# Performance work log

Measured on AMD Instinct MI355X. Metric: run time of the kernel, lower is better.

Reference implementation:

```python
import jax, jax.numpy as jnp
import numpy as np

NEG_INF_SCALE = -1e9


def setup_inputs() -> dict:
    key = jax.random.key(0)
    ks = jax.random.split(key, 8)
    B, T, M, D = 64, 1024, 256, 1024
    query = jax.random.normal(ks[0], (B, 1, M), dtype=jnp.float32)
    keys = jax.random.normal(ks[1], (B, T, M), dtype=jnp.float32)
    values = jax.random.normal(ks[2], (B, T, D), dtype=jnp.float32)
    mask = jax.random.randint(ks[3], (B, 1, T), 0, 2).astype(jnp.float32)
    # MLP params (scaled like torch default init ~ 1/sqrt(fan_in))
    W1 = jax.random.normal(ks[4], (4 * M, D), dtype=jnp.float32) / np.sqrt(4 * M)
    b1 = jnp.zeros((D,), dtype=jnp.float32)
    W2 = jax.random.normal(ks[5], (D, D), dtype=jnp.float32) / np.sqrt(D)
    b2 = jnp.zeros((D,), dtype=jnp.float32)
    w_score = jax.random.normal(ks[6], (D, 1), dtype=jnp.float32) / np.sqrt(D)
    b_score = jnp.zeros((1,), dtype=jnp.float32)
    return {"query": query, "keys": keys, "values": values, "mask": mask,
            "W1": W1, "b1": b1, "W2": W2, "b2": b2,
            "w_score": w_score, "b_score": b_score}


def reference(query, keys, values, mask, W1, b1, W2, b2, w_score, b_score):
    # query: [B,1,M] broadcast against keys: [B,T,M]
    q = jnp.broadcast_to(query, keys.shape)
    att_input = jnp.concatenate([q, keys, q - keys, q * keys], axis=-1)  # [B,T,4M]
    h = jax.nn.relu(att_input @ W1 + b1)   # [B,T,D]
    h = jax.nn.relu(h @ W2 + b2)           # [B,T,D]
    score = h @ w_score + b_score          # [B,T,1]
    logits = jnp.swapaxes(score, 1, 2)     # [B,1,T]
    logits = logits + mask * NEG_INF_SCALE
    attn = jax.nn.softmax(logits, axis=-1)  # [B,1,T]
    out = jnp.matmul(attn, values)          # [B,1,D]
    return out
```

## Files before the change

### kernel.cpp

```cpp
#include <hip/hip_runtime.h>

#define DEV __device__ __forceinline__

typedef __attribute__((ext_vector_type(4))) float f32x4;
typedef __attribute__((ext_vector_type(8))) short short8;
typedef __attribute__((ext_vector_type(4))) short s16x4;
typedef __attribute__((ext_vector_type(4))) float f32x4v;

DEV short f2bf(float f) {
  union { float f; unsigned u; } v; v.f = f;
  unsigned r = (v.u + 0x7FFFu + ((v.u >> 16) & 1u)) >> 16;
  return (short)r;
}

DEV void gload16(const void* g, void* l) {
  __builtin_amdgcn_global_load_lds(
      (const __attribute__((address_space(1))) void*)g,
      (__attribute__((address_space(3))) void*)l, 16, 0, 0);
}

#define BAR() __builtin_amdgcn_s_barrier()
#define LGKMW(n)                                              \
  {                                                           \
    asm volatile("s_waitcnt lgkmcnt(" #n ")" ::: "memory");   \
    __builtin_amdgcn_sched_barrier(0);                        \
  }
#define VMW(n)                                                \
  {                                                           \
    asm volatile("s_waitcnt vmcnt(" #n ")" ::: "memory");     \
    __builtin_amdgcn_sched_barrier(0);                        \
  }


__global__ __launch_bounds__(256) void k_prep_all(
    const float* __restrict__ keys, const float* __restrict__ w2,
    const float* __restrict__ w1, const float* __restrict__ query,
    const float* __restrict__ b1, short* __restrict__ keysb,
    short* __restrict__ w2f, short* __restrict__ wktf,
    float* __restrict__ biasb) {
  __shared__ __align__(16) char smem[45056];
  const int bid = blockIdx.x;
  const int tid = threadIdx.x;

  if (bid < 256) {
    short (*tile)[64][72] = (short (*)[64][72])(smem);
    float (*qlds)[256] = (float (*)[256])(smem + 36864);
    float (*redm)[64][4] = (float (*)[64][4])(smem + 40960);
    const int r = bid;
    const int bg = r & 15, d0g = r >> 4, d0 = d0g * 64;
    const int d = tid & 63, mq = tid >> 6;

    for (int idx = tid; idx < 1024; idx += 256)
      qlds[idx >> 8][idx & 255] = query[(bg * 4 + (idx >> 8)) * 256 + (idx & 255)];
    __syncthreads();

    float bacc[4] = {0.f, 0.f, 0.f, 0.f};
    const int l = tid & 63, cgl = tid >> 6;

    for (int mc = 0; mc < 4; ++mc) {
#pragma unroll 4
      for (int i = 0; i < 16; ++i) {
        int ml = i * 4 + mq;
        int m = mc * 64 + ml;
        float wa = w1[(size_t)m * 1024 + d0 + d];
        float wb = w1[(size_t)(256 + m) * 1024 + d0 + d];
        float wc = w1[(size_t)(512 + m) * 1024 + d0 + d];
        float wd = w1[(size_t)(768 + m) * 1024 + d0 + d];
        float bc = wb - wc, ac = wa + wc;
#pragma unroll
        for (int bb = 0; bb < 4; ++bb) {
          float qv = qlds[bb][m];
          tile[bb][d][ml] = f2bf(bc + qv * wd);
          bacc[bb] += qv * ac;
        }
      }
      __syncthreads();
#pragma unroll
      for (int bb = 0; bb < 4; ++bb) {
        short* ob = wktf + (size_t)(bg * 4 + bb) * 262144;
#pragma unroll
        for (int kh = 0; kh < 2; ++kh) {
          short8 v = *(const short8*)&tile[bb][cgl * 16 + (l & 15)]
                                          [kh * 32 + (l >> 4) * 8];
          *(short8*)&ob[((size_t)((mc * 2 + kh) * 64 + d0g * 4 + cgl)) * 512 + l * 8] = v;
        }
      }
      __syncthreads();
    }

    redm[0][d][mq] = bacc[0];
    redm[1][d][mq] = bacc[1];
    redm[2][d][mq] = bacc[2];
    redm[3][d][mq] = bacc[3];
    __syncthreads();
    const int bb = tid >> 6, dd = tid & 63;
    biasb[(bg * 4 + bb) * 1024 + d0 + dd] =
        redm[bb][dd][0] + redm[bb][dd][1] + redm[bb][dd][2] + redm[bb][dd][3] +
        b1[d0 + dd];
  } else if (bid < 512) {
    float (*tile)[65] = (float (*)[65])(smem);
    const int r = bid - 256;
    const int kt = r & 15, n0 = (r >> 4) * 64;
    const int a = tid & 63, q = tid >> 6;
#pragma unroll
    for (int i = 0; i < 16; ++i) {
      int kk = i * 4 + q;
      tile[kk][a] = w2[(size_t)(kt * 64 + kk) * 1024 + n0 + a];
    }
    __syncthreads();
    const int l = tid & 63, cgl = tid >> 6;
#pragma unroll
    for (int kh = 0; kh < 2; ++kh) {
      short8 v;
#pragma unroll
      for (int j = 0; j < 8; ++j)
        v[j] = f2bf(tile[kh * 32 + (l >> 4) * 8 + j][cgl * 16 + (l & 15)]);
      *(short8*)&w2f[((size_t)((kt * 2 + kh) * 64 + (n0 >> 4) + cgl)) * 512 + l * 8] = v;
    }
  } else {
    int i = ((bid - 512) * 256 + tid) * 8;
    f32x4v v0 = *(const f32x4v*)(keys + i);
    f32x4v v1 = *(const f32x4v*)(keys + i + 4);
    short8 s;
    s[0] = f2bf(v0[0]); s[1] = f2bf(v0[1]); s[2] = f2bf(v0[2]); s[3] = f2bf(v0[3]);
    s[4] = f2bf(v1[0]); s[5] = f2bf(v1[1]); s[6] = f2bf(v1[2]); s[7] = f2bf(v1[3]);
    *(short8*)(keysb + i) = s;
  }
}


template <int MODE>
__global__ __launch_bounds__(256, 3) void k_gemm(const short* __restrict__ A,
                                                 const short* __restrict__ Bf,
                                                 const float* __restrict__ bias,
                                                 const float* __restrict__ wscore,
                                                 short* __restrict__ hout,
                                                 float* __restrict__ spart) {
  __shared__ short lds[12288];
  constexpr int SK = (MODE == 1) ? 256 : 1024;
  constexpr int KT = (MODE == 1) ? 4 : 16;

  const int tid = threadIdx.x;
  const int bx = blockIdx.x;
  const int L = (bx & 7) * 512 + (bx >> 3);

  const short *Ab, *Bb;
  const float *biasp, *wsp = nullptr;
  short* houtp = nullptr;
  int rt, ct;
  if constexpr (MODE == 1) {
    const int b = L >> 6;
    rt = (L >> 2) & 15; ct = L & 3;
    Ab = A + ((size_t)(b * 1024 + rt * 64)) * 256;
    Bb = Bf + (size_t)b * 262144;
    biasp = bias + b * 1024 + ct * 256;
    houtp = hout + ((size_t)(b * 1024 + rt * 64)) * 1024 + ct * 256;
  } else {
    rt = L >> 2; ct = L & 3;
    Ab = A + (size_t)rt * 64 * 1024;
    Bb = Bf;
    biasp = bias + ct * 256;
    wsp = wscore + ct * 256;
  }

  int gA[2], dA[2];
#pragma unroll
  for (int j = 0; j < 2; ++j) {
    int s = tid + j * 256, row = s >> 3, kc = (s & 7) ^ (row & 7);
    gA[j] = row * SK + kc * 8;
    dA[j] = s * 8;
  }
  auto STAGE = [&](int kt) {
    const int bb = (kt % 3) * 4096;
#pragma unroll
    for (int j = 0; j < 2; ++j) gload16(Ab + gA[j] + kt * 64, &lds[bb + dA[j]]);
  };

  const int lane = tid & 63, l15 = lane & 15, l4 = lane >> 4, wc = tid >> 6;
  const int afo0 = l15 * 64 + ((l4 ^ (l15 & 7)) * 8);
  const int afo1 = l15 * 64 + (((4 + l4) ^ (l15 & 7)) * 8);

  f32x4 acc[4][4];
#pragma unroll
  for (int m = 0; m < 4; ++m)
#pragma unroll
    for (int n = 0; n < 4; ++n) acc[m][n] = f32x4{0.f, 0.f, 0.f, 0.f};
  short8 bf[4];
  short8 af[4];

#define LOADB(kt, kh_)                                                          \
  _Pragma("unroll") for (int n_ = 0; n_ < 4; ++n_) {                            \
    bf[n_] = *(const short8*)(Bb +                                              \
        ((size_t)(((kt) * 2 + (kh_)) * 64 + ct * 16 + wc * 4 + n_) << 9) +      \
        lane * 8);                                                              \
  }

  STAGE(0);
  STAGE(1);
  VMW(2);
  BAR();

#pragma unroll
  for (int t = 0; t < KT; ++t) {
    const int bb = (t % 3) * 4096;
    LOADB(t, 0);
#pragma unroll
    for (int m = 0; m < 4; ++m) af[m] = *(const short8*)&lds[bb + afo0 + m * 1024];
    LGKMW(0);
    __builtin_amdgcn_s_setprio(1);
#pragma unroll
    for (int m = 0; m < 4; ++m)
#pragma unroll
      for (int n = 0; n < 4; ++n)
        acc[m][n] = __builtin_amdgcn_mfma_f32_16x16x32_bf16(bf[n], af[m],
                                                            acc[m][n], 0, 0, 0);
    __builtin_amdgcn_s_setprio(0);
    LOADB(t, 1);
    if (t + 2 < KT) STAGE(t + 2);
#pragma unroll
    for (int m = 0; m < 4; ++m) af[m] = *(const short8*)&lds[bb + afo1 + m * 1024];
    LGKMW(0);
    __builtin_amdgcn_s_setprio(1);
#pragma unroll
    for (int m = 0; m < 4; ++m)
#pragma unroll
      for (int n = 0; n < 4; ++n)
        acc[m][n] = __builtin_amdgcn_mfma_f32_16x16x32_bf16(bf[n], af[m],
                                                            acc[m][n], 0, 0, 0);
    __builtin_amdgcn_s_setprio(0);
    if (t + 2 < KT) {
      VMW(2);
    } else {
      VMW(0);
    }
    BAR();
  }
#undef LOADB

  if constexpr (MODE == 1) {
    float bv[4][4];
#pragma unroll
    for (int n = 0; n < 4; ++n)
#pragma unroll
      for (int r2 = 0; r2 < 4; ++r2)
        bv[n][r2] = biasp[wc * 64 + n * 16 + l4 * 4 + r2];
#pragma unroll
    for (int m = 0; m < 4; ++m) {
      int row = m * 16 + l15;
#pragma unroll
      for (int n = 0; n < 4; ++n) {
        s16x4 pk;
#pragma unroll
        for (int r2 = 0; r2 < 4; ++r2)
          pk[r2] = f2bf(fmaxf(acc[m][n][r2] + bv[n][r2], 0.f));
        *(s16x4*)&houtp[(size_t)row * 1024 + wc * 64 + n * 16 + l4 * 4] = pk;
      }
    }
  } else {
    float bv[4][4], wv[4][4];
#pragma unroll
    for (int n = 0; n < 4; ++n)
#pragma unroll
      for (int r2 = 0; r2 < 4; ++r2) {
        int c = wc * 64 + n * 16 + l4 * 4 + r2;
        bv[n][r2] = biasp[c];
        wv[n][r2] = wsp[c];
      }
    float* so = spart + ((size_t)(ct * 4 + wc) << 16) + rt * 64;
#pragma unroll
    for (int m = 0; m < 4; ++m) {
      float s = 0.f;
#pragma unroll
      for (int n = 0; n < 4; ++n)
#pragma unroll
        for (int r2 = 0; r2 < 4; ++r2)
          s += fmaxf(acc[m][n][r2] + bv[n][r2], 0.f) * wv[n][r2];
      s += __shfl_xor(s, 16);
      s += __shfl_xor(s, 32);
      if (lane < 16) so[m * 16 + l15] = s;
    }
  }
}

__global__ __launch_bounds__(256) void k_out(const float* __restrict__ spart,
                                             const float* __restrict__ mask,
                                             const float* __restrict__ bscore,
                                             const float* __restrict__ values,
                                             float* __restrict__ part) {
  const int b = blockIdx.x >> 3, ts = blockIdx.x & 7;
  const int tid = threadIdx.x;
  __shared__ float sm[1024];
  __shared__ float red[8];
  const float bs = bscore[0];
  float lmax = -3.0e38f;
  for (int t = tid; t < 1024; t += 256) {
    float s = bs;
#pragma unroll
    for (int c = 0; c < 16; ++c) s += spart[(size_t)c * 65536 + b * 1024 + t];
    float lg = s + mask[b * 1024 + t] * (-1e9f);
    sm[t] = lg;
    lmax = fmaxf(lmax, lg);
  }
  for (int o = 32; o; o >>= 1) lmax = fmaxf(lmax, __shfl_xor(lmax, o));
  const int wid = tid >> 6, lane = tid & 63;
  if (lane == 0) red[wid] = lmax;
  __syncthreads();
  float bmax = fmaxf(fmaxf(red[0], red[1]), fmaxf(red[2], red[3]));
  float lsum = 0.f;
  for (int t = tid; t < 1024; t += 256) {
    float e = __expf(sm[t] - bmax);
    sm[t] = e;
    lsum += e;
  }
  for (int o = 32; o; o >>= 1) lsum += __shfl_xor(lsum, o);
  __syncthreads();
  if (lane == 0) red[wid] = lsum;
  __syncthreads();
  const float inv = 1.0f / (red[0] + red[1] + red[2] + red[3]);

  const float* vb = values + ((size_t)b * 1024 + ts * 128) * 1024 + tid * 4;
  f32x4 acc = {0.f, 0.f, 0.f, 0.f};
#pragma unroll 8
  for (int t = 0; t < 128; ++t) {
    f32x4v v = *(const f32x4v*)(vb + (size_t)t * 1024);
    float a = sm[ts * 128 + t] * inv;
    acc[0] += a * v[0]; acc[1] += a * v[1]; acc[2] += a * v[2]; acc[3] += a * v[3];
  }
  *(f32x4*)(part + ((size_t)(b * 8 + ts)) * 1024 + tid * 4) = acc;
}

__global__ __launch_bounds__(256) void k_red(const float* __restrict__ part,
                                             float* __restrict__ out) {
  const int b = blockIdx.x;
  const int c4 = threadIdx.x * 4;
  f32x4 s = {0.f, 0.f, 0.f, 0.f};
#pragma unroll
  for (int ts = 0; ts < 8; ++ts) {
    f32x4v v = *(const f32x4v*)(part + ((size_t)(b * 8 + ts)) * 1024 + c4);
    s[0] += v[0]; s[1] += v[1]; s[2] += v[2]; s[3] += v[3];
  }
  *(f32x4*)(out + b * 1024 + c4) = s;
}


extern "C" void kernel_launch(void* const* d_in, const int* in_sizes, int n_in,
                              void* d_out, int out_size, void* d_ws, size_t ws_size,
                              hipStream_t stream) {
  const float* query  = (const float*)d_in[0];
  const float* keys   = (const float*)d_in[1];
  const float* values = (const float*)d_in[2];
  const float* mask   = (const float*)d_in[3];
  const float* W1     = (const float*)d_in[4];
  const float* b1     = (const float*)d_in[5];
  const float* W2     = (const float*)d_in[6];
  const float* b2     = (const float*)d_in[7];
  const float* wscore = (const float*)d_in[8];
  const float* bscore = (const float*)d_in[9];
  float* out = (float*)d_out;

  char* ws = (char*)d_ws;
  short* keysb = (short*)(ws);
  short* wktf  = (short*)(ws + 33554432ull);
  short* w2f   = (short*)(ws + 67108864ull);
  float* biasb = (float*)(ws + 69206016ull);
  short* h1    = (short*)(ws + 69468160ull);
  float* spart = (float*)(ws + 203685888ull);
  float* part  = (float*)(ws + 207880192ull);

  k_prep_all<<<8704, 256, 0, stream>>>(keys, W2, W1, query, b1,
                                       keysb, w2f, wktf, biasb);

  k_gemm<1><<<4096, 256, 0, stream>>>(keysb, wktf, biasb, nullptr, h1, nullptr);
  k_gemm<2><<<4096, 256, 0, stream>>>(h1, w2f, b2, wscore, nullptr, spart);

  k_out<<<512, 256, 0, stream>>>(spart, mask, bscore, values, part);
  k_red<<<64, 256, 0, stream>>>(part, out);
}
```

Before: 269.6 us.

## Widen GEMM tiles to full 1024 columns with 8 waves and register double-buffered B

Each GEMM block now covers a 64x1024 output tile with 512 threads (8 waves, each owning 128 columns) instead of a 64x256 tile with 4 waves. The A tile is staged into LDS once per row block and shared across all columns, cutting redundant A reads by 4x. B fragments are double-buffered in registers, with next-k B loads issued ahead of compute. In the second GEMM the per-wave score partials are reduced in LDS and one score per row is written, which removes the 16-way partial sum from k_out. The trade-off is a larger accumulator (128 floats per lane) and more registers, which lowers occupancy, and only 1024 blocks are launched.

```diff
diff --git a/kernel.cpp b/kernel.cpp
--- a/kernel.cpp
+++ b/kernel.cpp
@@ -130,80 +130,71 @@
 
 
 template <int MODE>
-__global__ __launch_bounds__(256, 3) void k_gemm(const short* __restrict__ A,
-                                                 const short* __restrict__ Bf,
-                                                 const float* __restrict__ bias,
-                                                 const float* __restrict__ wscore,
-                                                 short* __restrict__ hout,
-                                                 float* __restrict__ spart) {
+__global__ __launch_bounds__(512, 2) void k_gemmw(const short* __restrict__ A,
+                                                  const short* __restrict__ Bf,
+                                                  const float* __restrict__ bias,
+                                                  const float* __restrict__ wscore,
+                                                  short* __restrict__ hout,
+                                                  float* __restrict__ score) {
   __shared__ short lds[12288];
+  __shared__ float red[8][64];
   constexpr int SK = (MODE == 1) ? 256 : 1024;
   constexpr int KT = (MODE == 1) ? 4 : 16;
 
   const int tid = threadIdx.x;
   const int bx = blockIdx.x;
-  const int L = (bx & 7) * 512 + (bx >> 3);
+  const int L = (bx & 7) * 128 + (bx >> 3);
 
   const short *Ab, *Bb;
   const float *biasp, *wsp = nullptr;
   short* houtp = nullptr;
-  int rt, ct;
   if constexpr (MODE == 1) {
-    const int b = L >> 6;
-    rt = (L >> 2) & 15; ct = L & 3;
-    Ab = A + ((size_t)(b * 1024 + rt * 64)) * 256;
+    const int b = L >> 4, rl = L & 15;
+    Ab = A + ((size_t)(b * 1024 + rl * 64)) * 256;
     Bb = Bf + (size_t)b * 262144;
-    biasp = bias + b * 1024 + ct * 256;
-    houtp = hout + ((size_t)(b * 1024 + rt * 64)) * 1024 + ct * 256;
+    biasp = bias + b * 1024;
+    houtp = hout + ((size_t)(b * 1024 + rl * 64)) * 1024;
   } else {
-    rt = L >> 2; ct = L & 3;
-    Ab = A + (size_t)rt * 64 * 1024;
+    Ab = A + (size_t)L * 64 * 1024;
     Bb = Bf;
-    biasp = bias + ct * 256;
-    wsp = wscore + ct * 256;
-  }
-
-  int gA[2], dA[2];
-#pragma unroll
-  for (int j = 0; j < 2; ++j) {
-    int s = tid + j * 256, row = s >> 3, kc = (s & 7) ^ (row & 7);
-    gA[j] = row * SK + kc * 8;
-    dA[j] = s * 8;
-  }
+    biasp = bias;
+    wsp = wscore;
+  }
+
+  const int srow = tid >> 3, skc = (tid & 7) ^ (srow & 7);
+  const int gA = srow * SK + skc * 8;
+  const int dA = tid * 8;
   auto STAGE = [&](int kt) {
-    const int bb = (kt % 3) * 4096;
-#pragma unroll
-    for (int j = 0; j < 2; ++j) gload16(Ab + gA[j] + kt * 64, &lds[bb + dA[j]]);
+    gload16(Ab + gA + kt * 64, &lds[(kt % 3) * 4096 + dA]);
   };
 
-  const int lane = tid & 63, l15 = lane & 15, l4 = lane >> 4, wc = tid >> 6;
+  const int lane = tid & 63, l15 = lane & 15, l4 = lane >> 4, w = tid >> 6;
   const int afo0 = l15 * 64 + ((l4 ^ (l15 & 7)) * 8);
   const int afo1 = l15 * 64 + (((4 + l4) ^ (l15 & 7)) * 8);
 
-  f32x4 acc[4][4];
+  f32x4 acc[4][8];
 #pragma unroll
   for (int m = 0; m < 4; ++m)
 #pragma unroll
-    for (int n = 0; n < 4; ++n) acc[m][n] = f32x4{0.f, 0.f, 0.f, 0.f};
-  short8 bf[4];
-  short8 af[4];
-
-#define LOADB(kt, kh_)                                                          \
-  _Pragma("unroll") for (int n_ = 0; n_ < 4; ++n_) {                            \
-    bf[n_] = *(const short8*)(Bb +                                              \
-        ((size_t)(((kt) * 2 + (kh_)) * 64 + ct * 16 + wc * 4 + n_) << 9) +      \
-        lane * 8);                                                              \
+    for (int n = 0; n < 8; ++n) acc[m][n] = f32x4{0.f, 0.f, 0.f, 0.f};
+  short8 bfA[8], bfB[8], af[4];
+
+#define LOADB(kt, kh_, BF)                                                      \
+  _Pragma("unroll") for (int n_ = 0; n_ < 8; ++n_) {                            \
+    BF[n_] = *(const short8*)(Bb +                                              \
+        ((size_t)(((kt) * 2 + (kh_)) * 64 + w * 8 + n_) << 9) + lane * 8);      \
   }
 
   STAGE(0);
+  LOADB(0, 0, bfA);
   STAGE(1);
-  VMW(2);
+  VMW(1);
   BAR();
 
 #pragma unroll
   for (int t = 0; t < KT; ++t) {
     const int bb = (t % 3) * 4096;
-    LOADB(t, 0);
+    LOADB(t, 1, bfB);
 #pragma unroll
     for (int m = 0; m < 4; ++m) af[m] = *(const short8*)&lds[bb + afo0 + m * 1024];
     LGKMW(0);
@@ -211,25 +202,27 @@
 #pragma unroll
     for (int m = 0; m < 4; ++m)
 #pragma unroll
-      for (int n = 0; n < 4; ++n)
-        acc[m][n] = __builtin_amdgcn_mfma_f32_16x16x32_bf16(bf[n], af[m],
+      for (int n = 0; n < 8; ++n)
+        acc[m][n] = __builtin_amdgcn_mfma_f32_16x16x32_bf16(bfA[n], af[m],
                                                             acc[m][n], 0, 0, 0);
     __builtin_amdgcn_s_setprio(0);
-    LOADB(t, 1);
+#pragma unroll
+    for (int m = 0; m < 4; ++m) af[m] = *(const short8*)&lds[bb + afo1 + m * 1024];
     if (t + 2 < KT) STAGE(t + 2);
-#pragma unroll
-    for (int m = 0; m < 4; ++m) af[m] = *(const short8*)&lds[bb + afo1 + m * 1024];
+    if (t + 1 < KT) LOADB(t + 1, 0, bfA);
     LGKMW(0);
     __builtin_amdgcn_s_setprio(1);
 #pragma unroll
     for (int m = 0; m < 4; ++m)
 #pragma unroll
-      for (int n = 0; n < 4; ++n)
-        acc[m][n] = __builtin_amdgcn_mfma_f32_16x16x32_bf16(bf[n], af[m],
+      for (int n = 0; n < 8; ++n)
+        acc[m][n] = __builtin_amdgcn_mfma_f32_16x16x32_bf16(bfB[n], af[m],
                                                             acc[m][n], 0, 0, 0);
     __builtin_amdgcn_s_setprio(0);
     if (t + 2 < KT) {
-      VMW(2);
+      VMW(9);
+    } else if (t + 1 < KT) {
+      VMW(8);
     } else {
       VMW(0);
     }
@@ -238,51 +231,50 @@
 #undef LOADB
 
   if constexpr (MODE == 1) {
-    float bv[4][4];
-#pragma unroll
-    for (int n = 0; n < 4; ++n)
+    float bv[8][4];
+#pragma unroll
+    for (int n = 0; n < 8; ++n)
 #pragma unroll
       for (int r2 = 0; r2 < 4; ++r2)
-        bv[n][r2] = biasp[wc * 64 + n * 16 + l4 * 4 + r2];
+        bv[n][r2] = biasp[w * 128 + n * 16 + l4 * 4 + r2];
 #pragma unroll
     for (int m = 0; m < 4; ++m) {
       int row = m * 16 + l15;
 #pragma unroll
-      for (int n = 0; n < 4; ++n) {
+      for (int n = 0; n < 8; ++n) {
         s16x4 pk;
 #pragma unroll
         for (int r2 = 0; r2 < 4; ++r2)
           pk[r2] = f2bf(fmaxf(acc[m][n][r2] + bv[n][r2], 0.f));
-        *(s16x4*)&houtp[(size_t)row * 1024 + wc * 64 + n * 16 + l4 * 4] = pk;
+        *(s16x4*)&houtp[(size_t)row * 1024 + w * 128 + n * 16 + l4 * 4] = pk;
       }
     }
   } else {
-    float bv[4][4], wv[4][4];
-#pragma unroll
-    for (int n = 0; n < 4; ++n)
-#pragma unroll
-      for (int r2 = 0; r2 < 4; ++r2) {
-        int c = wc * 64 + n * 16 + l4 * 4 + r2;
-        bv[n][r2] = biasp[c];
-        wv[n][r2] = wsp[c];
-      }
-    float* so = spart + ((size_t)(ct * 4 + wc) << 16) + rt * 64;
 #pragma unroll
     for (int m = 0; m < 4; ++m) {
       float s = 0.f;
 #pragma unroll
-      for (int n = 0; n < 4; ++n)
-#pragma unroll
-        for (int r2 = 0; r2 < 4; ++r2)
-          s += fmaxf(acc[m][n][r2] + bv[n][r2], 0.f) * wv[n][r2];
+      for (int n = 0; n < 8; ++n)
+#pragma unroll
+        for (int r2 = 0; r2 < 4; ++r2) {
+          int c = w * 128 + n * 16 + l4 * 4 + r2;
+          s += fmaxf(acc[m][n][r2] + biasp[c], 0.f) * wsp[c];
+        }
       s += __shfl_xor(s, 16);
       s += __shfl_xor(s, 32);
-      if (lane < 16) so[m * 16 + l15] = s;
-    }
-  }
-}
-
-__global__ __launch_bounds__(256) void k_out(const float* __restrict__ spart,
+      if (lane < 16) red[w][m * 16 + l15] = s;
+    }
+    __syncthreads();
+    if (tid < 64) {
+      float tsum = 0.f;
+#pragma unroll
+      for (int ww = 0; ww < 8; ++ww) tsum += red[ww][tid];
+      score[(size_t)L * 64 + tid] = tsum;
+    }
+  }
+}
+
+__global__ __launch_bounds__(256) void k_out(const float* __restrict__ score,
                                              const float* __restrict__ mask,
                                              const float* __restrict__ bscore,
                                              const float* __restrict__ values,
@@ -294,10 +286,7 @@
   const float bs = bscore[0];
   float lmax = -3.0e38f;
   for (int t = tid; t < 1024; t += 256) {
-    float s = bs;
-#pragma unroll
-    for (int c = 0; c < 16; ++c) s += spart[(size_t)c * 65536 + b * 1024 + t];
-    float lg = s + mask[b * 1024 + t] * (-1e9f);
+    float lg = score[b * 1024 + t] + bs + mask[b * 1024 + t] * (-1e9f);
     sm[t] = lg;
     lmax = fmaxf(lmax, lg);
   }
@@ -364,15 +353,15 @@
   short* w2f   = (short*)(ws + 67108864ull);
   float* biasb = (float*)(ws + 69206016ull);
   short* h1    = (short*)(ws + 69468160ull);
-  float* spart = (float*)(ws + 203685888ull);
+  float* score = (float*)(ws + 203685888ull);
   float* part  = (float*)(ws + 207880192ull);
 
   k_prep_all<<<8704, 256, 0, stream>>>(keys, W2, W1, query, b1,
                                        keysb, w2f, wktf, biasb);
 
-  k_gemm<1><<<4096, 256, 0, stream>>>(keysb, wktf, biasb, nullptr, h1, nullptr);
-  k_gemm<2><<<4096, 256, 0, stream>>>(h1, w2f, b2, wscore, nullptr, spart);
-
-  k_out<<<512, 256, 0, stream>>>(spart, mask, bscore, values, part);
+  k_gemmw<1><<<1024, 512, 0, stream>>>(keysb, wktf, biasb, nullptr, h1, nullptr);
+  k_gemmw<2><<<1024, 512, 0, stream>>>(h1, w2f, b2, wscore, nullptr, score);
+
+  k_out<<<512, 256, 0, stream>>>(score, mask, bscore, values, part);
   k_red<<<64, 256, 0, stream>>>(part, out);
 }
```

New measurement: 287.0 us. +6.4%, slower.

## Grow GEMM tiles to 128 rows with 8 waves and prefetch B fragments

Applied to the files above, without the earlier changes.

Both GEMM kernels now use 512-thread blocks that compute a 128x256 tile, with two wave rows sharing the same B fragments and a 4-slot LDS ring for A. B fragments for the next k-step are loaded one iteration ahead into double-buffered registers, so global B loads overlap the MFMA work. The grid is halved, which halves redundant B-matrix traffic per output row. In exchange, register and LDS use per block go up (64KB LDS, more VGPRs for bf), which may lower occupancy.

```diff
diff --git a/kernel.cpp b/kernel.cpp
--- a/kernel.cpp
+++ b/kernel.cpp
@@ -130,34 +130,34 @@
 
 
 template <int MODE>
-__global__ __launch_bounds__(256, 3) void k_gemm(const short* __restrict__ A,
+__global__ __launch_bounds__(512, 4) void k_gemm(const short* __restrict__ A,
                                                  const short* __restrict__ Bf,
                                                  const float* __restrict__ bias,
                                                  const float* __restrict__ wscore,
                                                  short* __restrict__ hout,
                                                  float* __restrict__ spart) {
-  __shared__ short lds[12288];
+  __shared__ short lds[32768];
   constexpr int SK = (MODE == 1) ? 256 : 1024;
   constexpr int KT = (MODE == 1) ? 4 : 16;
 
   const int tid = threadIdx.x;
   const int bx = blockIdx.x;
-  const int L = (bx & 7) * 512 + (bx >> 3);
+  const int L = (bx & 7) * 256 + (bx >> 3);
 
   const short *Ab, *Bb;
   const float *biasp, *wsp = nullptr;
   short* houtp = nullptr;
   int rt, ct;
   if constexpr (MODE == 1) {
-    const int b = L >> 6;
-    rt = (L >> 2) & 15; ct = L & 3;
-    Ab = A + ((size_t)(b * 1024 + rt * 64)) * 256;
+    const int b = L >> 5;
+    rt = (L >> 2) & 7; ct = L & 3;
+    Ab = A + ((size_t)(b * 1024 + rt * 128)) * 256;
     Bb = Bf + (size_t)b * 262144;
     biasp = bias + b * 1024 + ct * 256;
-    houtp = hout + ((size_t)(b * 1024 + rt * 64)) * 1024 + ct * 256;
+    houtp = hout + ((size_t)(b * 1024 + rt * 128)) * 1024 + ct * 256;
   } else {
     rt = L >> 2; ct = L & 3;
-    Ab = A + (size_t)rt * 64 * 1024;
+    Ab = A + (size_t)rt * 128 * 1024;
     Bb = Bf;
     biasp = bias + ct * 256;
     wsp = wscore + ct * 256;
@@ -166,44 +166,46 @@
   int gA[2], dA[2];
 #pragma unroll
   for (int j = 0; j < 2; ++j) {
-    int s = tid + j * 256, row = s >> 3, kc = (s & 7) ^ (row & 7);
+    int s = tid + j * 512, row = s >> 3, kc = (s & 7) ^ (row & 7);
     gA[j] = row * SK + kc * 8;
     dA[j] = s * 8;
   }
   auto STAGE = [&](int kt) {
-    const int bb = (kt % 3) * 4096;
+    const int bb = (kt & 3) * 8192;
 #pragma unroll
     for (int j = 0; j < 2; ++j) gload16(Ab + gA[j] + kt * 64, &lds[bb + dA[j]]);
   };
 
-  const int lane = tid & 63, l15 = lane & 15, l4 = lane >> 4, wc = tid >> 6;
-  const int afo0 = l15 * 64 + ((l4 ^ (l15 & 7)) * 8);
-  const int afo1 = l15 * 64 + (((4 + l4) ^ (l15 & 7)) * 8);
+  const int lane = tid & 63, l15 = lane & 15, l4 = lane >> 4;
+  const int wid = tid >> 6, wr = wid >> 2, wcc = wid & 3;
+  const int afo0 = wr * 4096 + l15 * 64 + ((l4 ^ (l15 & 7)) * 8);
+  const int afo1 = wr * 4096 + l15 * 64 + (((4 + l4) ^ (l15 & 7)) * 8);
 
   f32x4 acc[4][4];
 #pragma unroll
   for (int m = 0; m < 4; ++m)
 #pragma unroll
     for (int n = 0; n < 4; ++n) acc[m][n] = f32x4{0.f, 0.f, 0.f, 0.f};
-  short8 bf[4];
+  short8 bf[4][2];
   short8 af[4];
 
 #define LOADB(kt, kh_)                                                          \
   _Pragma("unroll") for (int n_ = 0; n_ < 4; ++n_) {                            \
-    bf[n_] = *(const short8*)(Bb +                                              \
-        ((size_t)(((kt) * 2 + (kh_)) * 64 + ct * 16 + wc * 4 + n_) << 9) +      \
+    bf[n_][kh_] = *(const short8*)(Bb +                                         \
+        ((size_t)(((kt) * 2 + (kh_)) * 64 + ct * 16 + wcc * 4 + n_) << 9) +     \
         lane * 8);                                                              \
   }
 
   STAGE(0);
+  LOADB(0, 0);
+  LOADB(0, 1);
   STAGE(1);
-  VMW(2);
+  VMW(10);
   BAR();
 
 #pragma unroll
   for (int t = 0; t < KT; ++t) {
-    const int bb = (t % 3) * 4096;
-    LOADB(t, 0);
+    const int bb = (t & 3) * 8192;
 #pragma unroll
     for (int m = 0; m < 4; ++m) af[m] = *(const short8*)&lds[bb + afo0 + m * 1024];
     LGKMW(0);
@@ -212,24 +214,27 @@
     for (int m = 0; m < 4; ++m)
 #pragma unroll
       for (int n = 0; n < 4; ++n)
-        acc[m][n] = __builtin_amdgcn_mfma_f32_16x16x32_bf16(bf[n], af[m],
+        acc[m][n] = __builtin_amdgcn_mfma_f32_16x16x32_bf16(bf[n][0], af[m],
                                                             acc[m][n], 0, 0, 0);
     __builtin_amdgcn_s_setprio(0);
-    LOADB(t, 1);
+    if (t + 1 < KT) LOADB(t + 1, 0);
+#pragma unroll
+    for (int m = 0; m < 4; ++m) af[m] = *(const short8*)&lds[bb + afo1 + m * 1024];
     if (t + 2 < KT) STAGE(t + 2);
-#pragma unroll
-    for (int m = 0; m < 4; ++m) af[m] = *(const short8*)&lds[bb + afo1 + m * 1024];
     LGKMW(0);
     __builtin_amdgcn_s_setprio(1);
 #pragma unroll
     for (int m = 0; m < 4; ++m)
 #pragma unroll
       for (int n = 0; n < 4; ++n)
-        acc[m][n] = __builtin_amdgcn_mfma_f32_16x16x32_bf16(bf[n], af[m],
+        acc[m][n] = __builtin_amdgcn_mfma_f32_16x16x32_bf16(bf[n][1], af[m],
                                                             acc[m][n], 0, 0, 0);
     __builtin_amdgcn_s_setprio(0);
+    if (t + 1 < KT) LOADB(t + 1, 1);
     if (t + 2 < KT) {
-      VMW(2);
+      VMW(10);
+    } else if (t + 1 < KT) {
+      VMW(8);
     } else {
       VMW(0);
     }
@@ -243,17 +248,17 @@
     for (int n = 0; n < 4; ++n)
 #pragma unroll
       for (int r2 = 0; r2 < 4; ++r2)
-        bv[n][r2] = biasp[wc * 64 + n * 16 + l4 * 4 + r2];
+        bv[n][r2] = biasp[wcc * 64 + n * 16 + l4 * 4 + r2];
 #pragma unroll
     for (int m = 0; m < 4; ++m) {
-      int row = m * 16 + l15;
+      int row = wr * 64 + m * 16 + l15;
 #pragma unroll
       for (int n = 0; n < 4; ++n) {
         s16x4 pk;
 #pragma unroll
         for (int r2 = 0; r2 < 4; ++r2)
           pk[r2] = f2bf(fmaxf(acc[m][n][r2] + bv[n][r2], 0.f));
-        *(s16x4*)&houtp[(size_t)row * 1024 + wc * 64 + n * 16 + l4 * 4] = pk;
+        *(s16x4*)&houtp[(size_t)row * 1024 + wcc * 64 + n * 16 + l4 * 4] = pk;
       }
     }
   } else {
@@ -262,11 +267,11 @@
     for (int n = 0; n < 4; ++n)
 #pragma unroll
       for (int r2 = 0; r2 < 4; ++r2) {
-        int c = wc * 64 + n * 16 + l4 * 4 + r2;
+        int c = wcc * 64 + n * 16 + l4 * 4 + r2;
         bv[n][r2] = biasp[c];
         wv[n][r2] = wsp[c];
       }
-    float* so = spart + ((size_t)(ct * 4 + wc) << 16) + rt * 64;
+    float* so = spart + ((size_t)(ct * 4 + wcc) << 16) + rt * 128 + wr * 64;
 #pragma unroll
     for (int m = 0; m < 4; ++m) {
       float s = 0.f;
@@ -370,8 +375,8 @@
   k_prep_all<<<8704, 256, 0, stream>>>(keys, W2, W1, query, b1,
                                        keysb, w2f, wktf, biasb);
 
-  k_gemm<1><<<4096, 256, 0, stream>>>(keysb, wktf, biasb, nullptr, h1, nullptr);
-  k_gemm<2><<<4096, 256, 0, stream>>>(h1, w2f, b2, wscore, nullptr, spart);
+  k_gemm<1><<<2048, 512, 0, stream>>>(keysb, wktf, biasb, nullptr, h1, nullptr);
+  k_gemm<2><<<2048, 512, 0, stream>>>(h1, w2f, b2, wscore, nullptr, spart);
 
   k_out<<<512, 256, 0, stream>>>(spart, mask, bscore, values, part);
   k_red<<<64, 256, 0, stream>>>(part, out);
```

After: 271.6 us. Within noise of the previous version (+0.7%).
